# Kernel optimization log

Hardware: AMD Instinct MI355X
Metric: run time of the kernel (lower is better)

Reference implementation:

```python
import jax, jax.numpy as jnp
import numpy as np

B, Q, D, H, HD = 16, 300, 256, 8, 32
LV, P, NL, FF, NC = 3, 4, 6, 1024, 80
SPATIAL = ((80, 80), (40, 40), (20, 20))
LEN = sum(h * w for h, w in SPATIAL)  # 8400


def _layer_norm(x, g, b):
    m = jnp.mean(x, -1, keepdims=True)
    v = jnp.mean((x - m) ** 2, -1, keepdims=True)
    return (x - m) * jax.lax.rsqrt(v + 1e-5) * g + b


def _inverse_sigmoid(x, eps=1e-5):
    x = jnp.clip(x, eps, 1.0 - eps)
    return jnp.log(x / (1.0 - x))


def _bilinear(img, x, y, Hl, Wl):
    # img: (B*H, C, Hl*Wl); x, y: (B*H, N) pixel coords; matches
    # F.grid_sample(align_corners=False, padding_mode='zeros')
    x0 = jnp.floor(x)
    y0 = jnp.floor(y)
    wx1 = x - x0
    wy1 = y - y0

    def g(xi, yi, w):
        valid = (xi >= 0) & (xi <= Wl - 1) & (yi >= 0) & (yi <= Hl - 1)
        idx = jnp.clip(yi, 0, Hl - 1).astype(jnp.int32) * Wl + jnp.clip(xi, 0, Wl - 1).astype(jnp.int32)
        idxb = jnp.broadcast_to(idx[:, None, :], (img.shape[0], img.shape[1], idx.shape[-1]))
        v = jnp.take_along_axis(img, idxb, axis=2)
        return v * (w * valid)[:, None, :]

    return (g(x0, y0, (1 - wx1) * (1 - wy1)) + g(x0 + 1, y0, wx1 * (1 - wy1))
            + g(x0, y0 + 1, (1 - wx1) * wy1) + g(x0 + 1, y0 + 1, wx1 * wy1))


def _msda(query, ref, value, oW, ob, aW, ab, OW, Ob):
    # query: (B,Q,D); ref: (B,Q,4) in [0,1]; value: (B,LEN,H,HD)
    off = (query @ oW + ob).reshape(B, Q, H, LV, P, 2)
    aw = jax.nn.softmax((query @ aW + ab).reshape(B, Q, H, LV * P), -1).reshape(B, Q, H, LV, P)
    loc = ref[:, :, None, None, None, :2] + off / P * ref[:, :, None, None, None, 2:] * 0.5
    out = jnp.zeros((B, Q, H, HD), query.dtype)
    start = 0
    for l, (Hl, Wl) in enumerate(SPATIAL):
        img = value[:, start:start + Hl * Wl].transpose(0, 2, 3, 1).reshape(B * H, HD, Hl * Wl)
        start += Hl * Wl
        gl = loc[:, :, :, l].transpose(0, 2, 1, 3, 4).reshape(B * H, Q * P, 2)
        s = _bilinear(img, gl[..., 0] * Wl - 0.5, gl[..., 1] * Hl - 0.5, Hl, Wl).reshape(B, H, HD, Q, P)
        out = out + jnp.einsum('bhdqp,bqhp->bqhd', s, aw[:, :, :, l])
    return out.reshape(B, Q, D) @ OW + Ob


def _mha(qx, kx, vx, Wq, bq, Wk, bk, Wv, bv, Wo, bo):
    q = (qx @ Wq + bq).reshape(B, Q, H, HD)
    k = (kx @ Wk + bk).reshape(B, Q, H, HD)
    v = (vx @ Wv + bv).reshape(B, Q, H, HD)
    a = jax.nn.softmax(jnp.einsum('bqhd,bkhd->bhqk', q, k) * np.float32(1.0 / np.sqrt(HD)), -1)
    return jnp.einsum('bhqk,bkhd->bqhd', a, v).reshape(B, Q, D) @ Wo + bo


def _core(tgt, ref_points_unact, memory, self_Wq, self_bq, self_Wk, self_bk, self_Wv, self_bv, self_Wo, self_bo, ln1_g, ln1_b, ln2_g, ln2_b, ln3_g, ln3_b, off_W, off_b, aw_W, aw_b, val_W, val_b, out_W, out_b, ffn_W1, ffn_b1, ffn_W2, ffn_b2, qph_W1, qph_b1, qph_W2, qph_b2, bb_W1, bb_b1, bb_W2, bb_b2, bb_W3, bb_b3, sc_W, sc_b):
    out = tgt
    ref = jax.nn.sigmoid(ref_points_unact)
    for i in range(NL):
        qpe = jax.nn.relu(ref @ qph_W1 + qph_b1) @ qph_W2 + qph_b2
        q = out + qpe
        out = _layer_norm(out + _mha(q, q, out, self_Wq[i], self_bq[i], self_Wk[i], self_bk[i], self_Wv[i], self_bv[i], self_Wo[i], self_bo[i]), ln1_g[i], ln1_b[i])
        value = (memory @ val_W[i] + val_b[i]).reshape(B, LEN, H, HD)
        out = _layer_norm(out + _msda(out + qpe, ref, value, off_W[i], off_b[i], aw_W[i], aw_b[i], out_W[i], out_b[i]), ln2_g[i], ln2_b[i])
        ff = jax.nn.relu(out @ ffn_W1[i] + ffn_b1[i]) @ ffn_W2[i] + ffn_b2[i]
        out = _layer_norm(out + ff, ln3_g[i], ln3_b[i])
        bb = jax.nn.relu(out @ bb_W1[i] + bb_b1[i])
        bb = jax.nn.relu(bb @ bb_W2[i] + bb_b2[i])
        bb = bb @ bb_W3[i] + bb_b3[i]
        ref = jax.nn.sigmoid(bb + _inverse_sigmoid(ref))
    logits = out @ sc_W[NL - 1] + sc_b[NL - 1]
    return ref, logits


def setup_inputs():
    ks = iter(jax.random.split(jax.random.key(0), 48))

    def rn(shape, s=0.02):
        return jax.random.normal(next(ks), shape, jnp.float32) * s

    z = lambda shape: jnp.zeros(shape, jnp.float32)
    o = lambda shape: jnp.ones(shape, jnp.float32)
    L = NL
    return {
        'tgt': rn((B, Q, D), 1.0),
        'ref_points_unact': rn((B, Q, 4), 1.0),
        'memory': rn((B, LEN, D), 1.0),
        'memory_spatial_shapes': jnp.array(SPATIAL, jnp.int32),
        'self_Wq': rn((L, D, D)), 'self_bq': z((L, D)),
        'self_Wk': rn((L, D, D)), 'self_bk': z((L, D)),
        'self_Wv': rn((L, D, D)), 'self_bv': z((L, D)),
        'self_Wo': rn((L, D, D)), 'self_bo': z((L, D)),
        'ln1_g': o((L, D)), 'ln1_b': z((L, D)),
        'ln2_g': o((L, D)), 'ln2_b': z((L, D)),
        'ln3_g': o((L, D)), 'ln3_b': z((L, D)),
        'off_W': rn((L, D, H * LV * P * 2)), 'off_b': rn((L, H * LV * P * 2), 0.5),
        'aw_W': rn((L, D, H * LV * P)), 'aw_b': z((L, H * LV * P)),
        'val_W': rn((L, D, D)), 'val_b': z((L, D)),
        'out_W': rn((L, D, D)), 'out_b': z((L, D)),
        'ffn_W1': rn((L, D, FF)), 'ffn_b1': z((L, FF)),
        'ffn_W2': rn((L, FF, D)), 'ffn_b2': z((L, D)),
        'qph_W1': rn((4, 2 * D)), 'qph_b1': z((2 * D,)),
        'qph_W2': rn((2 * D, D)), 'qph_b2': z((D,)),
        'bb_W1': rn((L, D, D)), 'bb_b1': z((L, D)),
        'bb_W2': rn((L, D, D)), 'bb_b2': z((L, D)),
        'bb_W3': rn((L, D, 4)), 'bb_b3': z((L, 4)),
        'sc_W': rn((L, D, NC)), 'sc_b': z((L, NC)),
    }


def reference(tgt, ref_points_unact, memory, memory_spatial_shapes, self_Wq, self_bq, self_Wk, self_bk, self_Wv, self_bv, self_Wo, self_bo, ln1_g, ln1_b, ln2_g, ln2_b, ln3_g, ln3_b, off_W, off_b, aw_W, aw_b, val_W, val_b, out_W, out_b, ffn_W1, ffn_b1, ffn_W2, ffn_b2, qph_W1, qph_b1, qph_W2, qph_b2, bb_W1, bb_b1, bb_W2, bb_b2, bb_W3, bb_b3, sc_W, sc_b):
    # memory_spatial_shapes must equal SPATIAL (static constants under jit)
    ref, logits = _core(tgt, ref_points_unact, memory, self_Wq, self_bq, self_Wk, self_bk, self_Wv, self_bv, self_Wo, self_bo, ln1_g, ln1_b, ln2_g, ln2_b, ln3_g, ln3_b, off_W, off_b, aw_W, aw_b, val_W, val_b, out_W, out_b, ffn_W1, ffn_b1, ffn_W2, ffn_b2, qph_W1, qph_b1, qph_W2, qph_b2, bb_W1, bb_b1, bb_W2, bb_b2, bb_W3, bb_b3, sc_W, sc_b)
    # eval path: stacked outputs from the eval_idx (last) layer
    return (ref[None], logits[None])
```

## Files before the change

kernel.cpp:

```cpp
#include <hip/hip_runtime.h>

#define DI __device__ __forceinline__

typedef __attribute__((ext_vector_type(8))) short short8;
typedef __attribute__((ext_vector_type(4))) float f32x4;
typedef unsigned short u16;

DI u16 f2bf(float f) {
    union { float f; unsigned u; } v; v.f = f;
    unsigned u = v.u;
    return (u16)((u + 0x7fffu + ((u >> 16) & 1u)) >> 16);
}
DI float bf2f(u16 h) {
    union { unsigned u; float f; } v; v.u = ((unsigned)h) << 16;
    return v.f;
}
DI int lds_off(int row, int slot) {
    return row * 64 + (((slot ^ ((row >> 1) & 3)) << 4));
}

__global__ __launch_bounds__(256) void k_wt(const float* __restrict__ W, u16* __restrict__ Wt,
                                            int K, int N, int dstL)
{
    __shared__ u16 t[32][33];
    const int tid = threadIdx.x;
    const int kt = blockIdx.x * 32, nt = blockIdx.y * 32;
    const float* Wl = W + (size_t)blockIdx.z * K * N;
    u16* Wtl = Wt + (size_t)blockIdx.z * dstL;
#pragma unroll
    for (int i = 0; i < 4; i++) {
        int k = kt + (tid >> 5) + i * 8;
        int n = nt + (tid & 31);
        float v = (n < N) ? Wl[(size_t)k * N + n] : 0.f;
        t[tid & 31][(tid >> 5) + i * 8] = f2bf(v);
    }
    __syncthreads();
#pragma unroll
    for (int i = 0; i < 4; i++) {
        int n = nt + (tid >> 5) + i * 8;
        int k = kt + (tid & 31);
        if (n < N) Wtl[(size_t)n * K + k] = t[(tid >> 5) + i * 8][tid & 31];
    }
}

__global__ void k_packbias(const float* __restrict__ a, const float* __restrict__ b,
                           int na, int nb, float* __restrict__ dst)
{
    int i = blockIdx.x * 256 + threadIdx.x;
    int L = blockIdx.z;
    float* d = dst + (size_t)L * (na + nb);
    if (i < na) d[i] = a[(size_t)L * na + i];
    if (i < nb) d[na + i] = b[(size_t)L * nb + i];
}

template<int TM, int AMODE, int STORE, bool RELU, bool RESID>
__global__ __launch_bounds__(256) void k_gemm(
    const void* __restrict__ Ap, const float* __restrict__ A2,
    const u16* __restrict__ Bt, const float* __restrict__ bias,
    const float* __restrict__ resid, void* __restrict__ Cp,
    int M, int N, int K)
{
    constexpr int MI = TM / 32;
    __shared__ alignas(16) char Asm[TM * 64];
    __shared__ alignas(16) char Bsm[128 * 64];
    const int tid  = threadIdx.x;
    const int lane = tid & 63;
    const int wave = tid >> 6;
    const int wr = wave >> 1, wc = wave & 1;
    const int m0 = blockIdx.x * TM, n0 = blockIdx.y * 128;

    f32x4 acc[MI][4] = {};

    for (int kb = 0; kb < K; kb += 32) {
        if (AMODE == 2) {
            const u16* A = (const u16*)Ap;
            int r = tid >> 2, ko = (tid & 3) << 3;
            int grow = m0 + r; if (grow > M - 1) grow = M - 1;
            uint4 v = *(const uint4*)(A + (size_t)grow * K + kb + ko);
            *(uint4*)(Asm + lds_off(r, ko >> 3)) = v;
        } else {
            constexpr int AIT = (TM * 8) / 256;
#pragma unroll
            for (int j = 0; j < AIT; j++) {
                int flat = tid + j * 256;
                int r = flat >> 3, kq = flat & 7;
                int grow = m0 + r; if (grow > M - 1) grow = M - 1;
                const float* p = (const float*)Ap + (size_t)grow * K + kb + (kq << 2);
                float4 v = *(const float4*)p;
                if (AMODE == 1) {
                    float4 w = *(const float4*)(A2 + (size_t)grow * K + kb + (kq << 2));
                    v.x += w.x; v.y += w.y; v.z += w.z; v.w += w.w;
                }
                ushort4 h; h.x = f2bf(v.x); h.y = f2bf(v.y); h.z = f2bf(v.z); h.w = f2bf(v.w);
                *(ushort4*)(Asm + lds_off(r, kq >> 1) + ((kq & 1) << 3)) = h;
            }
        }
#pragma unroll
        for (int j = 0; j < 2; j++) {
            int item = tid + j * 256;
            int n = item >> 2, kq = item & 3;
            int gn = n0 + n; if (gn > N - 1) gn = N - 1;
            uint4 v = *(const uint4*)(Bt + (size_t)gn * K + kb + (kq << 3));
            *(uint4*)(Bsm + lds_off(n, kq)) = v;
        }
        __syncthreads();

        short8 af[MI], bfr[4];
#pragma unroll
        for (int mi = 0; mi < MI; mi++) {
            int r = wr * (TM / 2) + (mi << 4) + (lane & 15);
            af[mi] = *(const short8*)(Asm + lds_off(r, lane >> 4));
        }
#pragma unroll
        for (int ni = 0; ni < 4; ni++) {
            int c = (wc << 6) + (ni << 4) + (lane & 15);
            bfr[ni] = *(const short8*)(Bsm + lds_off(c, lane >> 4));
        }
#pragma unroll
        for (int mi = 0; mi < MI; mi++)
#pragma unroll
            for (int ni = 0; ni < 4; ni++)
                acc[mi][ni] = __builtin_amdgcn_mfma_f32_16x16x32_bf16(af[mi], bfr[ni], acc[mi][ni], 0, 0, 0);
        __syncthreads();
    }

    const int cl = lane & 15, rb = (lane >> 4) << 2;
#pragma unroll
    for (int mi = 0; mi < MI; mi++) {
#pragma unroll
        for (int ni = 0; ni < 4; ni++) {
            int col = n0 + (wc << 6) + (ni << 4) + cl;
            if (col >= N) continue;
            float bv = bias[col];
#pragma unroll
            for (int e = 0; e < 4; e++) {
                int row = m0 + wr * (TM / 2) + (mi << 4) + rb + e;
                if (row >= M) continue;
                float v = acc[mi][ni][e] + bv;
                if (RESID) v += resid[(size_t)row * N + col];
                if (RELU)  v = fmaxf(v, 0.f);
                if (STORE == 0) {
                    ((float*)Cp)[(size_t)row * N + col] = v;
                } else {
                    int b = row / 8400, pix = row - b * 8400;
                    int h = col >> 5, hd = col & 31;
                    ((u16*)Cp)[(((size_t)(b * 8 + h)) * 8400 + pix) * 32 + hd] = f2bf(v);
                }
            }
        }
    }
}

__global__ __launch_bounds__(256) void k_mha3(const float* __restrict__ qk, const float* __restrict__ Vp,
                                              float* __restrict__ outp)
{
    __shared__ alignas(16) char lds[62976];
    u16* Ksh = (u16*)lds;
    u16* Psh = (u16*)lds;
    u16* Vt  = (u16*)(lds + 41984);

    const int q0 = blockIdx.x * 64;
    const int bh = blockIdx.y;
    const int h = bh & 7, b = bh >> 3;
    const int tid = threadIdx.x;
    const int wv = tid >> 6, l = tid & 63;
    const int c15 = l & 15, slot = l >> 4;
    const float scale = 0.17677669529663687f;

    for (int item = tid; item < 304 * 8; item += 256) {
        int kk = item >> 3, dq = (item & 7) << 2;
        ushort4 hv = {0, 0, 0, 0};
        if (kk < 300) {
            float4 v = *(const float4*)(qk + (size_t)(b * 300 + kk) * 512 + 256 + h * 32 + dq);
            hv.x = f2bf(v.x); hv.y = f2bf(v.y); hv.z = f2bf(v.z); hv.w = f2bf(v.w);
        }
        *(ushort4*)(Ksh + kk * 40 + dq) = hv;
    }
    for (int item = tid; item < 320 * 8; item += 256) {
        int kk = item >> 3, dq = (item & 7) << 2;
        float4 v = {0, 0, 0, 0};
        if (kk < 300)
            v = *(const float4*)(Vp + (size_t)(b * 300 + kk) * 256 + h * 32 + dq);
        Vt[(dq + 0) * 328 + kk] = f2bf(v.x);
        Vt[(dq + 1) * 328 + kk] = f2bf(v.y);
        Vt[(dq + 2) * 328 + kk] = f2bf(v.z);
        Vt[(dq + 3) * 328 + kk] = f2bf(v.w);
    }
    short8 qf;
    {
        int qrow = q0 + 16 * wv + c15; if (qrow > 299) qrow = 299;
        const float* qs = qk + (size_t)(b * 300 + qrow) * 512 + h * 32 + (slot << 3);
        float4 a0 = *(const float4*)qs, a1 = *(const float4*)(qs + 4);
        qf[0] = (short)f2bf(a0.x * scale); qf[1] = (short)f2bf(a0.y * scale);
        qf[2] = (short)f2bf(a0.z * scale); qf[3] = (short)f2bf(a0.w * scale);
        qf[4] = (short)f2bf(a1.x * scale); qf[5] = (short)f2bf(a1.y * scale);
        qf[6] = (short)f2bf(a1.z * scale); qf[7] = (short)f2bf(a1.w * scale);
    }
    __syncthreads();

    f32x4 sc[19];
    const f32x4 zero4 = {0.f, 0.f, 0.f, 0.f};
#pragma unroll
    for (int t = 0; t < 19; t++) {
        short8 kf = *(const short8*)(Ksh + (16 * t + c15) * 40 + (slot << 3));
        sc[t] = __builtin_amdgcn_mfma_f32_16x16x32_bf16(qf, kf, zero4, 0, 0, 0);
    }
    __syncthreads();

    float linv[4];
    const int prow0 = 16 * wv + (slot << 2);
#pragma unroll
    for (int e = 0; e < 4; e++) {
        float mm = -1e30f;
#pragma unroll
        for (int t = 0; t < 18; t++) mm = fmaxf(mm, sc[t][e]);
        if (c15 < 12) mm = fmaxf(mm, sc[18][e]);
        mm = fmaxf(mm, __shfl_xor(mm, 1));
        mm = fmaxf(mm, __shfl_xor(mm, 2));
        mm = fmaxf(mm, __shfl_xor(mm, 4));
        mm = fmaxf(mm, __shfl_xor(mm, 8));
        float ls = 0.f;
#pragma unroll
        for (int t = 0; t < 19; t++) {
            float p = __expf(sc[t][e] - mm);
            if (t == 18 && c15 >= 12) p = 0.f;
            ls += p;
            Psh[(prow0 + e) * 328 + 16 * t + c15] = f2bf(p);
        }
        ls += __shfl_xor(ls, 1);
        ls += __shfl_xor(ls, 2);
        ls += __shfl_xor(ls, 4);
        ls += __shfl_xor(ls, 8);
        linv[e] = 1.f / ls;
    }
    {
        int r = 16 * wv + (l >> 2);
        int c = 304 + ((l & 3) << 2);
        Psh[r * 328 + c + 0] = 0; Psh[r * 328 + c + 1] = 0;
        Psh[r * 328 + c + 2] = 0; Psh[r * 328 + c + 3] = 0;
    }

#pragma unroll
    for (int df = 0; df < 2; df++) {
        f32x4 o = zero4;
#pragma unroll
        for (int t = 0; t < 10; t++) {
            short8 pf = *(const short8*)(Psh + (16 * wv + c15) * 328 + 32 * t + (slot << 3));
            short8 vf = *(const short8*)(Vt + (16 * df + c15) * 328 + 32 * t + (slot << 3));
            o = __builtin_amdgcn_mfma_f32_16x16x32_bf16(pf, vf, o, 0, 0, 0);
        }
#pragma unroll
        for (int e = 0; e < 4; e++) {
            int qrow = q0 + prow0 + e;
            if (qrow < 300)
                outp[(size_t)(b * 300 + qrow) * 256 + h * 32 + 16 * df + c15] = o[e] * linv[e];
        }
    }
}

__global__ __launch_bounds__(256) void k_ln(const float* __restrict__ x, const float* __restrict__ g,
                                            const float* __restrict__ bb, float* __restrict__ out, int M)
{
    int row = blockIdx.x * 4 + (threadIdx.x >> 6);
    int lane = threadIdx.x & 63;
    if (row >= M) return;
    const float* xr = x + (size_t)row * 256;
    float4 v = *(const float4*)(xr + lane * 4);
    float s  = v.x + v.y + v.z + v.w;
    float s2 = v.x*v.x + v.y*v.y + v.z*v.z + v.w*v.w;
#pragma unroll
    for (int off = 32; off >= 1; off >>= 1) {
        s  += __shfl_xor(s, off);
        s2 += __shfl_xor(s2, off);
    }
    float m   = s * 0.00390625f;
    float var = s2 * 0.00390625f - m * m;
    float r   = rsqrtf(var + 1e-5f);
    float4 gv = *(const float4*)(g + lane * 4);
    float4 bv = *(const float4*)(bb + lane * 4);
    float4 o;
    o.x = (v.x - m) * r * gv.x + bv.x;
    o.y = (v.y - m) * r * gv.y + bv.y;
    o.z = (v.z - m) * r * gv.z + bv.z;
    o.w = (v.w - m) * r * gv.w + bv.w;
    *(float4*)(out + (size_t)row * 256 + lane * 4) = o;
}

__global__ void k_awsm(float* __restrict__ offaw, int n)
{
    int g = blockIdx.x * 256 + threadIdx.x;
    if (g >= n) return;
    int row = g >> 3, h = g & 7;
    float* p = offaw + (size_t)row * 288 + 192 + h * 12;
    float m = p[0];
#pragma unroll
    for (int i = 1; i < 12; i++) m = fmaxf(m, p[i]);
    float e[12]; float s = 0.f;
#pragma unroll
    for (int i = 0; i < 12; i++) { e[i] = __expf(p[i] - m); s += e[i]; }
    float inv = 1.f / s;
#pragma unroll
    for (int i = 0; i < 12; i++) p[i] = e[i] * inv;
}

__global__ __launch_bounds__(256) void k_msda(const u16* __restrict__ value, const float* __restrict__ offaw,
                                              const float* __restrict__ ref, float* __restrict__ samp)
{
    int it = blockIdx.x * 8 + (threadIdx.x >> 5);
    int d  = threadIdx.x & 31;
    int h = it & 7, row = it >> 3;
    int b = row / 300;
    const float* rf = ref + (size_t)row * 4;
    float rx = rf[0], ry = rf[1];
    float rw = rf[2] * 0.125f, rh = rf[3] * 0.125f;
    const float* offp = offaw + (size_t)row * 288 + h * 24;
    const float* awp  = offaw + (size_t)row * 288 + 192 + h * 12;
    const u16* vb = value + ((size_t)(b * 8 + h)) * 8400 * 32 + d;
    const int HW[3] = {80, 40, 20};
    const int st[3] = {0, 6400, 8000};
    float acc = 0.f;
#pragma unroll
    for (int lv = 0; lv < 3; lv++) {
        int Wl = HW[lv], Hl = HW[lv];
        float Wf = (float)Wl, Hf = (float)Hl;
#pragma unroll
        for (int p = 0; p < 4; p++) {
            float a = awp[lv * 4 + p];
            float x = (rx + offp[lv*8 + p*2]     * rw) * Wf - 0.5f;
            float y = (ry + offp[lv*8 + p*2 + 1] * rh) * Hf - 0.5f;
            float xf = floorf(x), yf = floorf(y);
            float wx = x - xf, wy = y - yf;
            int x0 = (int)xf, y0 = (int)yf;
#pragma unroll
            for (int t = 0; t < 4; t++) {
                int xx = x0 + (t & 1), yy = y0 + (t >> 1);
                if (xx >= 0 && xx < Wl && yy >= 0 && yy < Hl) {
                    float w = ((t & 1) ? wx : 1.f - wx) * ((t >> 1) ? wy : 1.f - wy);
                    acc += a * w * bf2f(vb[(size_t)(st[lv] + yy * Wl + xx) * 32]);
                }
            }
        }
    }
    samp[(size_t)row * 256 + h * 32 + d] = acc;
}

__global__ void k_qpe_hidden(const float* __restrict__ ref, const float* __restrict__ W1,
                             const float* __restrict__ b1, float* __restrict__ hid)
{
    int idx = blockIdx.x * 256 + threadIdx.x;
    if (idx >= 4800 * 512) return;
    int row = idx >> 9, col = idx & 511;
    const float* r = ref + (size_t)row * 4;
    float v = b1[col] + r[0]*W1[col] + r[1]*W1[512+col] + r[2]*W1[1024+col] + r[3]*W1[1536+col];
    hid[idx] = fmaxf(v, 0.f);
}

__global__ __launch_bounds__(64) void k_bb3(const float* __restrict__ bb2, const float* __restrict__ W3,
                                            const float* __restrict__ b3, float* __restrict__ ref)
{
    int row = blockIdx.x;
    int lane = threadIdx.x;
    const float* xr = bb2 + (size_t)row * 256;
    float s0 = 0, s1 = 0, s2 = 0, s3 = 0;
#pragma unroll
    for (int k = lane; k < 256; k += 64) {
        float xv = xr[k];
        float4 w = *(const float4*)(W3 + k * 4);
        s0 += xv * w.x; s1 += xv * w.y; s2 += xv * w.z; s3 += xv * w.w;
    }
#pragma unroll
    for (int off = 32; off >= 1; off >>= 1) {
        s0 += __shfl_xor(s0, off); s1 += __shfl_xor(s1, off);
        s2 += __shfl_xor(s2, off); s3 += __shfl_xor(s3, off);
    }
    if (lane == 0) {
        float sv[4] = {s0, s1, s2, s3};
        float* rr = ref + (size_t)row * 4;
#pragma unroll
        for (int j = 0; j < 4; j++) {
            float v = sv[j] + b3[j];
            float o = rr[j];
            o = fminf(fmaxf(o, 1e-5f), 1.f - 1e-5f);
            float inv = logf(o / (1.f - o));
            rr[j] = 1.f / (1.f + expf(-(v + inv)));
        }
    }
}

__global__ void k_cvt_bf16(const float* __restrict__ in, u16* __restrict__ out, int n4)
{
    int i = blockIdx.x * 256 + threadIdx.x;
    if (i >= n4) return;
    float4 v = ((const float4*)in)[i];
    ushort4 h; h.x = f2bf(v.x); h.y = f2bf(v.y); h.z = f2bf(v.z); h.w = f2bf(v.w);
    ((ushort4*)out)[i] = h;
}
__global__ void k_copy4(const float* __restrict__ in, float* __restrict__ out, int n4)
{
    int i = blockIdx.x * 256 + threadIdx.x;
    if (i >= n4) return;
    ((float4*)out)[i] = ((const float4*)in)[i];
}
__global__ void k_sigmoid(const float* __restrict__ in, float* __restrict__ out, int n)
{
    int i = blockIdx.x * 256 + threadIdx.x;
    if (i >= n) return;
    out[i] = 1.f / (1.f + __expf(-in[i]));
}

static inline dim3 g32(int M, int N) { return dim3((M + 31) / 32, (N + 127) / 128); }

static void gemm_plain(const float* A, const u16* Bt, const float* bias, float* C,
                       int M, int N, int K, hipStream_t s) {
    k_gemm<32, 0, 0, false, false><<<g32(M, N), 256, 0, s>>>((const void*)A, nullptr, Bt, bias, nullptr, (void*)C, M, N, K);
}
static void gemm_add(const float* A, const float* A2, const u16* Bt, const float* bias, float* C,
                     int M, int N, int K, hipStream_t s) {
    k_gemm<32, 1, 0, false, false><<<g32(M, N), 256, 0, s>>>((const void*)A, A2, Bt, bias, nullptr, (void*)C, M, N, K);
}
static void gemm_resid(const float* A, const u16* Bt, const float* bias, const float* resid, float* C,
                       int M, int N, int K, hipStream_t s) {
    k_gemm<32, 0, 0, false, true><<<g32(M, N), 256, 0, s>>>((const void*)A, nullptr, Bt, bias, resid, (void*)C, M, N, K);
}
static void gemm_relu(const float* A, const u16* Bt, const float* bias, float* C,
                      int M, int N, int K, hipStream_t s) {
    k_gemm<32, 0, 0, true, false><<<g32(M, N), 256, 0, s>>>((const void*)A, nullptr, Bt, bias, nullptr, (void*)C, M, N, K);
}
static void gemm_value(const u16* A, const u16* Bt, const float* bias, u16* C, hipStream_t s) {
    k_gemm<64, 2, 1, false, false><<<dim3(2100, 2), 256, 0, s>>>((const void*)A, nullptr, Bt, bias, nullptr, (void*)C, 134400, 256, 256);
}

extern "C" void kernel_launch(void* const* d_in, const int* in_sizes, int n_in,
                              void* d_out, int out_size, void* d_ws, size_t ws_size,
                              hipStream_t stream)
{
    const float* tgt       = (const float*)d_in[0];
    const float* ref_unact = (const float*)d_in[1];
    const float* memory    = (const float*)d_in[2];
    const float* self_Wq = (const float*)d_in[4];
    const float* self_bq = (const float*)d_in[5];
    const float* self_Wk = (const float*)d_in[6];
    const float* self_bk = (const float*)d_in[7];
    const float* self_Wv = (const float*)d_in[8];
    const float* self_bv = (const float*)d_in[9];
    const float* self_Wo = (const float*)d_in[10];
    const float* self_bo = (const float*)d_in[11];
    const float* ln1_g = (const float*)d_in[12];
    const float* ln1_b = (const float*)d_in[13];
    const float* ln2_g = (const float*)d_in[14];
    const float* ln2_b = (const float*)d_in[15];
    const float* ln3_g = (const float*)d_in[16];
    const float* ln3_b = (const float*)d_in[17];
    const float* off_W = (const float*)d_in[18];
    const float* off_b = (const float*)d_in[19];
    const float* aw_W  = (const float*)d_in[20];
    const float* aw_b  = (const float*)d_in[21];
    const float* val_W = (const float*)d_in[22];
    const float* val_b = (const float*)d_in[23];
    const float* out_W = (const float*)d_in[24];
    const float* out_b = (const float*)d_in[25];
    const float* ffn_W1 = (const float*)d_in[26];
    const float* ffn_b1 = (const float*)d_in[27];
    const float* ffn_W2 = (const float*)d_in[28];
    const float* ffn_b2 = (const float*)d_in[29];
    const float* qph_W1 = (const float*)d_in[30];
    const float* qph_b1 = (const float*)d_in[31];
    const float* qph_W2 = (const float*)d_in[32];
    const float* qph_b2 = (const float*)d_in[33];
    const float* bb_W1 = (const float*)d_in[34];
    const float* bb_b1 = (const float*)d_in[35];
    const float* bb_W2 = (const float*)d_in[36];
    const float* bb_b2 = (const float*)d_in[37];
    const float* bb_W3 = (const float*)d_in[38];
    const float* bb_b3 = (const float*)d_in[39];
    const float* sc_W  = (const float*)d_in[40];
    const float* sc_b  = (const float*)d_in[41];
    float* out_f = (float*)d_out;

    char* w = (char*)d_ws;
    u16* mem_bf = (u16*)(w + 0);
    u16* value  = (u16*)(w + 68812800);
    const size_t F0 = 137625600;
    float* ws_out   = (float*)(w + F0);
    float* ws_tmp   = (float*)(w + F0 +  4915200);
    float* ws_qpe   = (float*)(w + F0 +  9830400);
    float* ws_hid   = (float*)(w + F0 + 14745600);
    float* ws_qk    = (float*)(w + F0 + 24576000);
    float* ws_v     = (float*)(w + F0 + 34406400);
    float* ws_attn  = (float*)(w + F0 + 39321600);
    float* ws_offaw = (float*)(w + F0 + 44236800);
    float* ws_samp  = (float*)(w + F0 + 49766400);
    float* ws_ffn   = (float*)(w + F0 + 54681600);
    float* ws_bb1   = (float*)(w + F0 + 74342400);
    float* ws_bb2   = (float*)(w + F0 + 79257600);
    float* ws_ref   = (float*)(w + F0 + 84172800);
    float* bias_qk  = (float*)(w + F0 + 84256800);
    float* bias_oa  = (float*)(w + F0 + 84269088);
    u16* wt = (u16*)(w + F0 + 84276000);
    u16* wt_qk    = wt;
    u16* wt_v     = wt_qk    + 786432;
    u16* wt_o     = wt_v     + 393216;
    u16* wt_offaw = wt_o     + 393216;
    u16* wt_val   = wt_offaw + 442368;
    u16* wt_out   = wt_val   + 393216;
    u16* wt_f1    = wt_out   + 393216;
    u16* wt_f2    = wt_f1    + 1572864;
    u16* wt_b1    = wt_f2    + 1572864;
    u16* wt_b2    = wt_b1    + 393216;
    u16* wt_qp2   = wt_b2    + 393216;
    u16* wt_sc    = wt_qp2   + 131072;

    k_wt<<<dim3(8, 8, 6),  256, 0, stream>>>(self_Wq, wt_qk,            256, 256, 131072);
    k_wt<<<dim3(8, 8, 6),  256, 0, stream>>>(self_Wk, wt_qk + 65536,    256, 256, 131072);
    k_wt<<<dim3(8, 8, 6),  256, 0, stream>>>(self_Wv, wt_v,             256, 256, 65536);
    k_wt<<<dim3(8, 8, 6),  256, 0, stream>>>(self_Wo, wt_o,             256, 256, 65536);
    k_wt<<<dim3(8, 6, 6),  256, 0, stream>>>(off_W,   wt_offaw,         256, 192, 73728);
    k_wt<<<dim3(8, 3, 6),  256, 0, stream>>>(aw_W,    wt_offaw + 49152, 256, 96,  73728);
    k_wt<<<dim3(8, 8, 6),  256, 0, stream>>>(val_W,   wt_val,           256, 256, 65536);
    k_wt<<<dim3(8, 8, 6),  256, 0, stream>>>(out_W,   wt_out,           256, 256, 65536);
    k_wt<<<dim3(8, 32, 6), 256, 0, stream>>>(ffn_W1,  wt_f1,            256, 1024, 262144);
    k_wt<<<dim3(32, 8, 6), 256, 0, stream>>>(ffn_W2,  wt_f2,            1024, 256, 262144);
    k_wt<<<dim3(8, 8, 6),  256, 0, stream>>>(bb_W1,   wt_b1,            256, 256, 65536);
    k_wt<<<dim3(8, 8, 6),  256, 0, stream>>>(bb_W2,   wt_b2,            256, 256, 65536);
    k_wt<<<dim3(16, 8, 1), 256, 0, stream>>>(qph_W2,  wt_qp2,           512, 256, 131072);
    k_wt<<<dim3(8, 3, 1),  256, 0, stream>>>(sc_W + (size_t)5 * 20480, wt_sc, 256, 80, 20480);
    k_packbias<<<dim3(1, 1, 6), 256, 0, stream>>>(self_bq, self_bk, 256, 256, bias_qk);
    k_packbias<<<dim3(1, 1, 6), 256, 0, stream>>>(off_b, aw_b, 192, 96, bias_oa);

    k_cvt_bf16<<<33600, 256, 0, stream>>>(memory, mem_bf, 8601600);
    k_copy4   <<<1200,  256, 0, stream>>>(tgt, ws_out, 307200);
    k_sigmoid <<<75,    256, 0, stream>>>(ref_unact, ws_ref, 19200);

    for (int l = 0; l < 6; l++) {
        k_qpe_hidden<<<9600, 256, 0, stream>>>(ws_ref, qph_W1, qph_b1, ws_hid);
        gemm_plain(ws_hid, wt_qp2, qph_b2, ws_qpe, 4800, 256, 512, stream);

        gemm_add(ws_out, ws_qpe, wt_qk + (size_t)l * 131072, bias_qk + l * 512, ws_qk, 4800, 512, 256, stream);
        gemm_plain(ws_out, wt_v + (size_t)l * 65536, self_bv + l * 256, ws_v, 4800, 256, 256, stream);
        k_mha3<<<dim3(5, 128), 256, 0, stream>>>(ws_qk, ws_v, ws_attn);
        gemm_resid(ws_attn, wt_o + (size_t)l * 65536, self_bo + l * 256, ws_out, ws_tmp, 4800, 256, 256, stream);
        k_ln<<<1200, 256, 0, stream>>>(ws_tmp, ln1_g + l * 256, ln1_b + l * 256, ws_out, 4800);

        gemm_value(mem_bf, wt_val + (size_t)l * 65536, val_b + l * 256, value, stream);

        gemm_add(ws_out, ws_qpe, wt_offaw + (size_t)l * 73728, bias_oa + l * 288, ws_offaw, 4800, 288, 256, stream);
        k_awsm<<<150, 256, 0, stream>>>(ws_offaw, 38400);
        k_msda<<<4800, 256, 0, stream>>>(value, ws_offaw, ws_ref, ws_samp);
        gemm_resid(ws_samp, wt_out + (size_t)l * 65536, out_b + l * 256, ws_out, ws_tmp, 4800, 256, 256, stream);
        k_ln<<<1200, 256, 0, stream>>>(ws_tmp, ln2_g + l * 256, ln2_b + l * 256, ws_out, 4800);

        gemm_relu(ws_out, wt_f1 + (size_t)l * 262144, ffn_b1 + l * 1024, ws_ffn, 4800, 1024, 256, stream);
        gemm_resid(ws_ffn, wt_f2 + (size_t)l * 262144, ffn_b2 + l * 256, ws_out, ws_tmp, 4800, 256, 1024, stream);
        k_ln<<<1200, 256, 0, stream>>>(ws_tmp, ln3_g + l * 256, ln3_b + l * 256, ws_out, 4800);

        gemm_relu(ws_out, wt_b1 + (size_t)l * 65536, bb_b1 + l * 256, ws_bb1, 4800, 256, 256, stream);
        gemm_relu(ws_bb1, wt_b2 + (size_t)l * 65536, bb_b2 + l * 256, ws_bb2, 4800, 256, 256, stream);
        k_bb3<<<4800, 64, 0, stream>>>(ws_bb2, bb_W3 + (size_t)l * 1024, bb_b3 + l * 4, ws_ref);
    }

    k_copy4<<<19, 256, 0, stream>>>(ws_ref, out_f, 4800);
    gemm_plain(ws_out, wt_sc, sc_b + 5 * 80, out_f + 19200, 4800, 80, 256, stream);
}
```

Baseline: 2.208 ms.

## Fuse QKV projection, GEMM+residual+LayerNorm, softmax into MSDA; enlarge value-GEMM tile

Measured after the change: 2.333 ms. 5.7% more time.

```diff
diff --git a/kernel.cpp b/kernel.cpp
--- a/kernel.cpp
+++ b/kernel.cpp
@@ -43,14 +43,12 @@
     }
 }
 
-__global__ void k_packbias(const float* __restrict__ a, const float* __restrict__ b,
-                           int na, int nb, float* __restrict__ dst)
+__global__ void k_packb(const float* __restrict__ src, int n, float* __restrict__ dst,
+                        int off, int dstL)
 {
     int i = blockIdx.x * 256 + threadIdx.x;
     int L = blockIdx.z;
-    float* d = dst + (size_t)L * (na + nb);
-    if (i < na) d[i] = a[(size_t)L * na + i];
-    if (i < nb) d[na + i] = b[(size_t)L * nb + i];
+    if (i < n) dst[(size_t)L * dstL + off + i] = src[(size_t)L * n + i];
 }
 
 template<int TM, int AMODE, int STORE, bool RELU, bool RESID>
@@ -68,16 +66,21 @@
     const int wave = tid >> 6;
     const int wr = wave >> 1, wc = wave & 1;
     const int m0 = blockIdx.x * TM, n0 = blockIdx.y * 128;
+    const bool addA2 = (AMODE == 1) || (AMODE == 3 && n0 < 512);
 
     f32x4 acc[MI][4] = {};
 
     for (int kb = 0; kb < K; kb += 32) {
         if (AMODE == 2) {
             const u16* A = (const u16*)Ap;
-            int r = tid >> 2, ko = (tid & 3) << 3;
-            int grow = m0 + r; if (grow > M - 1) grow = M - 1;
-            uint4 v = *(const uint4*)(A + (size_t)grow * K + kb + ko);
-            *(uint4*)(Asm + lds_off(r, ko >> 3)) = v;
+#pragma unroll
+            for (int j = 0; j < (TM * 4) / 256; j++) {
+                int item = tid + j * 256;
+                int r = item >> 2, ko = (item & 3) << 3;
+                int grow = m0 + r; if (grow > M - 1) grow = M - 1;
+                uint4 v = *(const uint4*)(A + (size_t)grow * K + kb + ko);
+                *(uint4*)(Asm + lds_off(r, ko >> 3)) = v;
+            }
         } else {
             constexpr int AIT = (TM * 8) / 256;
 #pragma unroll
@@ -87,7 +90,7 @@
                 int grow = m0 + r; if (grow > M - 1) grow = M - 1;
                 const float* p = (const float*)Ap + (size_t)grow * K + kb + (kq << 2);
                 float4 v = *(const float4*)p;
-                if (AMODE == 1) {
+                if (addA2) {
                     float4 w = *(const float4*)(A2 + (size_t)grow * K + kb + (kq << 2));
                     v.x += w.x; v.y += w.y; v.z += w.z; v.w += w.w;
                 }
@@ -151,8 +154,94 @@
     }
 }
 
-__global__ __launch_bounds__(256) void k_mha3(const float* __restrict__ qk, const float* __restrict__ Vp,
-                                              float* __restrict__ outp)
+__global__ __launch_bounds__(256) void k_gemm_ln(
+    const float* __restrict__ Ap, const u16* __restrict__ Bt, const float* __restrict__ bias,
+    const float* __restrict__ resid, const float* __restrict__ g, const float* __restrict__ bb,
+    float* __restrict__ outp, int M, int K)
+{
+    __shared__ alignas(16) char lds[17408];
+    char* Asm = lds;
+    char* Bsm = lds + 1024;
+    float* Cf = (float*)lds;
+    const int tid = threadIdx.x;
+    const int lane = tid & 63;
+    const int wc = tid >> 6;
+    const int c15 = lane & 15, slot = lane >> 4;
+    const int m0 = blockIdx.x * 16;
+
+    f32x4 acc[4] = {};
+
+    for (int kb = 0; kb < K; kb += 32) {
+        if (tid < 128) {
+            int r = tid >> 3, kq = tid & 7;
+            const float* p = Ap + (size_t)(m0 + r) * K + kb + (kq << 2);
+            float4 v = *(const float4*)p;
+            ushort4 h; h.x = f2bf(v.x); h.y = f2bf(v.y); h.z = f2bf(v.z); h.w = f2bf(v.w);
+            *(ushort4*)(Asm + lds_off(r, kq >> 1) + ((kq & 1) << 3)) = h;
+        }
+#pragma unroll
+        for (int j = 0; j < 4; j++) {
+            int item = tid + j * 256;
+            int n = item >> 2, kq = item & 3;
+            uint4 v = *(const uint4*)(Bt + (size_t)n * K + kb + (kq << 3));
+            *(uint4*)(Bsm + lds_off(n, kq)) = v;
+        }
+        __syncthreads();
+
+        short8 af = *(const short8*)(Asm + lds_off(c15, slot));
+#pragma unroll
+        for (int ni = 0; ni < 4; ni++) {
+            int c = (wc << 6) + (ni << 4) + c15;
+            short8 bfr = *(const short8*)(Bsm + lds_off(c, slot));
+            acc[ni] = __builtin_amdgcn_mfma_f32_16x16x32_bf16(af, bfr, acc[ni], 0, 0, 0);
+        }
+        __syncthreads();
+    }
+
+#pragma unroll
+    for (int ni = 0; ni < 4; ni++) {
+        int col = (wc << 6) + (ni << 4) + c15;
+        float bv = bias[col];
+#pragma unroll
+        for (int e = 0; e < 4; e++) {
+            int rowl = (slot << 2) + e;
+            float v = acc[ni][e] + bv + resid[(size_t)(m0 + rowl) * 256 + col];
+            Cf[rowl * 264 + col] = v;
+        }
+    }
+    __syncthreads();
+
+    const int row = tid >> 4, l16 = tid & 15;
+    float s = 0.f, s2 = 0.f;
+#pragma unroll
+    for (int j = 0; j < 16; j++) {
+        float x = Cf[row * 264 + l16 + j * 16];
+        s += x; s2 += x * x;
+    }
+    s  += __shfl_xor(s, 1);  s2 += __shfl_xor(s2, 1);
+    s  += __shfl_xor(s, 2);  s2 += __shfl_xor(s2, 2);
+    s  += __shfl_xor(s, 4);  s2 += __shfl_xor(s2, 4);
+    s  += __shfl_xor(s, 8);  s2 += __shfl_xor(s2, 8);
+    float m   = s * 0.00390625f;
+    float var = s2 * 0.00390625f - m * m;
+    float r   = rsqrtf(var + 1e-5f);
+    float* orow = outp + (size_t)(m0 + row) * 256;
+#pragma unroll
+    for (int j = 0; j < 4; j++) {
+        int c = j * 64 + l16 * 4;
+        float4 x = *(const float4*)(Cf + row * 264 + c);
+        float4 gv = *(const float4*)(g + c);
+        float4 bv = *(const float4*)(bb + c);
+        float4 o;
+        o.x = (x.x - m) * r * gv.x + bv.x;
+        o.y = (x.y - m) * r * gv.y + bv.y;
+        o.z = (x.z - m) * r * gv.z + bv.z;
+        o.w = (x.w - m) * r * gv.w + bv.w;
+        *(float4*)(orow + c) = o;
+    }
+}
+
+__global__ __launch_bounds__(256) void k_mha3(const float* __restrict__ qkv, float* __restrict__ outp)
 {
     __shared__ alignas(16) char lds[62976];
     u16* Ksh = (u16*)lds;
@@ -171,7 +260,7 @@
         int kk = item >> 3, dq = (item & 7) << 2;
         ushort4 hv = {0, 0, 0, 0};
         if (kk < 300) {
-            float4 v = *(const float4*)(qk + (size_t)(b * 300 + kk) * 512 + 256 + h * 32 + dq);
+            float4 v = *(const float4*)(qkv + (size_t)(b * 300 + kk) * 768 + 256 + h * 32 + dq);
             hv.x = f2bf(v.x); hv.y = f2bf(v.y); hv.z = f2bf(v.z); hv.w = f2bf(v.w);
         }
         *(ushort4*)(Ksh + kk * 40 + dq) = hv;
@@ -180,7 +269,7 @@
         int kk = item >> 3, dq = (item & 7) << 2;
         float4 v = {0, 0, 0, 0};
         if (kk < 300)
-            v = *(const float4*)(Vp + (size_t)(b * 300 + kk) * 256 + h * 32 + dq);
+            v = *(const float4*)(qkv + (size_t)(b * 300 + kk) * 768 + 512 + h * 32 + dq);
         Vt[(dq + 0) * 328 + kk] = f2bf(v.x);
         Vt[(dq + 1) * 328 + kk] = f2bf(v.y);
         Vt[(dq + 2) * 328 + kk] = f2bf(v.z);
@@ -189,7 +278,7 @@
     short8 qf;
     {
         int qrow = q0 + 16 * wv + c15; if (qrow > 299) qrow = 299;
-        const float* qs = qk + (size_t)(b * 300 + qrow) * 512 + h * 32 + (slot << 3);
+        const float* qs = qkv + (size_t)(b * 300 + qrow) * 768 + h * 32 + (slot << 3);
         float4 a0 = *(const float4*)qs, a1 = *(const float4*)(qs + 4);
         qf[0] = (short)f2bf(a0.x * scale); qf[1] = (short)f2bf(a0.y * scale);
         qf[2] = (short)f2bf(a0.z * scale); qf[3] = (short)f2bf(a0.w * scale);
@@ -256,51 +345,6 @@
                 outp[(size_t)(b * 300 + qrow) * 256 + h * 32 + 16 * df + c15] = o[e] * linv[e];
         }
     }
-}
-
-__global__ __launch_bounds__(256) void k_ln(const float* __restrict__ x, const float* __restrict__ g,
-                                            const float* __restrict__ bb, float* __restrict__ out, int M)
-{
-    int row = blockIdx.x * 4 + (threadIdx.x >> 6);
-    int lane = threadIdx.x & 63;
-    if (row >= M) return;
-    const float* xr = x + (size_t)row * 256;
-    float4 v = *(const float4*)(xr + lane * 4);
-    float s  = v.x + v.y + v.z + v.w;
-    float s2 = v.x*v.x + v.y*v.y + v.z*v.z + v.w*v.w;
-#pragma unroll
-    for (int off = 32; off >= 1; off >>= 1) {
-        s  += __shfl_xor(s, off);
-        s2 += __shfl_xor(s2, off);
-    }
-    float m   = s * 0.00390625f;
-    float var = s2 * 0.00390625f - m * m;
-    float r   = rsqrtf(var + 1e-5f);
-    float4 gv = *(const float4*)(g + lane * 4);
-    float4 bv = *(const float4*)(bb + lane * 4);
-    float4 o;
-    o.x = (v.x - m) * r * gv.x + bv.x;
-    o.y = (v.y - m) * r * gv.y + bv.y;
-    o.z = (v.z - m) * r * gv.z + bv.z;
-    o.w = (v.w - m) * r * gv.w + bv.w;
-    *(float4*)(out + (size_t)row * 256 + lane * 4) = o;
-}
-
-__global__ void k_awsm(float* __restrict__ offaw, int n)
-{
-    int g = blockIdx.x * 256 + threadIdx.x;
-    if (g >= n) return;
-    int row = g >> 3, h = g & 7;
-    float* p = offaw + (size_t)row * 288 + 192 + h * 12;
-    float m = p[0];
-#pragma unroll
-    for (int i = 1; i < 12; i++) m = fmaxf(m, p[i]);
-    float e[12]; float s = 0.f;
-#pragma unroll
-    for (int i = 0; i < 12; i++) { e[i] = __expf(p[i] - m); s += e[i]; }
-    float inv = 1.f / s;
-#pragma unroll
-    for (int i = 0; i < 12; i++) p[i] = e[i] * inv;
 }
 
 __global__ __launch_bounds__(256) void k_msda(const u16* __restrict__ value, const float* __restrict__ offaw,
@@ -315,6 +359,18 @@
     float rw = rf[2] * 0.125f, rh = rf[3] * 0.125f;
     const float* offp = offaw + (size_t)row * 288 + h * 24;
     const float* awp  = offaw + (size_t)row * 288 + 192 + h * 12;
+    float aw[12];
+    {
+        float mm = awp[0];
+#pragma unroll
+        for (int i = 1; i < 12; i++) mm = fmaxf(mm, awp[i]);
+        float ssum = 0.f;
+#pragma unroll
+        for (int i = 0; i < 12; i++) { aw[i] = __expf(awp[i] - mm); ssum += aw[i]; }
+        float inv = 1.f / ssum;
+#pragma unroll
+        for (int i = 0; i < 12; i++) aw[i] *= inv;
+    }
     const u16* vb = value + ((size_t)(b * 8 + h)) * 8400 * 32 + d;
     const int HW[3] = {80, 40, 20};
     const int st[3] = {0, 6400, 8000};
@@ -325,7 +381,7 @@
         float Wf = (float)Wl, Hf = (float)Hl;
 #pragma unroll
         for (int p = 0; p < 4; p++) {
-            float a = awp[lv * 4 + p];
+            float a = aw[lv * 4 + p];
             float x = (rx + offp[lv*8 + p*2]     * rw) * Wf - 0.5f;
             float y = (ry + offp[lv*8 + p*2 + 1] * rh) * Hf - 0.5f;
             float xf = floorf(x), yf = floorf(y);
@@ -418,16 +474,20 @@
                      int M, int N, int K, hipStream_t s) {
     k_gemm<32, 1, 0, false, false><<<g32(M, N), 256, 0, s>>>((const void*)A, A2, Bt, bias, nullptr, (void*)C, M, N, K);
 }
-static void gemm_resid(const float* A, const u16* Bt, const float* bias, const float* resid, float* C,
-                       int M, int N, int K, hipStream_t s) {
-    k_gemm<32, 0, 0, false, true><<<g32(M, N), 256, 0, s>>>((const void*)A, nullptr, Bt, bias, resid, (void*)C, M, N, K);
+static void gemm_qkv(const float* A, const float* A2, const u16* Bt, const float* bias, float* C,
+                     hipStream_t s) {
+    k_gemm<32, 3, 0, false, false><<<g32(4800, 768), 256, 0, s>>>((const void*)A, A2, Bt, bias, nullptr, (void*)C, 4800, 768, 256);
 }
 static void gemm_relu(const float* A, const u16* Bt, const float* bias, float* C,
                       int M, int N, int K, hipStream_t s) {
     k_gemm<32, 0, 0, true, false><<<g32(M, N), 256, 0, s>>>((const void*)A, nullptr, Bt, bias, nullptr, (void*)C, M, N, K);
 }
 static void gemm_value(const u16* A, const u16* Bt, const float* bias, u16* C, hipStream_t s) {
-    k_gemm<64, 2, 1, false, false><<<dim3(2100, 2), 256, 0, s>>>((const void*)A, nullptr, Bt, bias, nullptr, (void*)C, 134400, 256, 256);
+    k_gemm<128, 2, 1, false, false><<<dim3(1050, 2), 256, 0, s>>>((const void*)A, nullptr, Bt, bias, nullptr, (void*)C, 134400, 256, 256);
+}
+static void gemm_ln(const float* A, const u16* Bt, const float* bias, const float* resid,
+                    const float* g, const float* bb, float* out, int K, hipStream_t s) {
+    k_gemm_ln<<<300, 256, 0, s>>>(A, Bt, bias, resid, g, bb, out, 4800, K);
 }
 
 extern "C" void kernel_launch(void* const* d_in, const int* in_sizes, int n_in,
@@ -482,24 +542,21 @@
     u16* value  = (u16*)(w + 68812800);
     const size_t F0 = 137625600;
     float* ws_out   = (float*)(w + F0);
-    float* ws_tmp   = (float*)(w + F0 +  4915200);
-    float* ws_qpe   = (float*)(w + F0 +  9830400);
-    float* ws_hid   = (float*)(w + F0 + 14745600);
-    float* ws_qk    = (float*)(w + F0 + 24576000);
-    float* ws_v     = (float*)(w + F0 + 34406400);
-    float* ws_attn  = (float*)(w + F0 + 39321600);
-    float* ws_offaw = (float*)(w + F0 + 44236800);
-    float* ws_samp  = (float*)(w + F0 + 49766400);
-    float* ws_ffn   = (float*)(w + F0 + 54681600);
-    float* ws_bb1   = (float*)(w + F0 + 74342400);
-    float* ws_bb2   = (float*)(w + F0 + 79257600);
-    float* ws_ref   = (float*)(w + F0 + 84172800);
-    float* bias_qk  = (float*)(w + F0 + 84256800);
-    float* bias_oa  = (float*)(w + F0 + 84269088);
-    u16* wt = (u16*)(w + F0 + 84276000);
-    u16* wt_qk    = wt;
-    u16* wt_v     = wt_qk    + 786432;
-    u16* wt_o     = wt_v     + 393216;
+    float* ws_qpe   = (float*)(w + F0 +  4915200);
+    float* ws_hid   = (float*)(w + F0 +  9830400);
+    float* ws_qkv   = (float*)(w + F0 + 19660800);
+    float* ws_attn  = (float*)(w + F0 + 34406400);
+    float* ws_offaw = (float*)(w + F0 + 39321600);
+    float* ws_samp  = (float*)(w + F0 + 44851200);
+    float* ws_ffn   = (float*)(w + F0 + 49766400);
+    float* ws_bb1   = (float*)(w + F0 + 69427200);
+    float* ws_bb2   = (float*)(w + F0 + 74342400);
+    float* ws_ref   = (float*)(w + F0 + 79257600);
+    float* bias_qkv = (float*)(w + F0 + 79334400);
+    float* bias_oa  = (float*)(w + F0 + 79352832);
+    u16* wt = (u16*)(w + F0 + 79360000);
+    u16* wt_qkv   = wt;
+    u16* wt_o     = wt_qkv   + 1179648;
     u16* wt_offaw = wt_o     + 393216;
     u16* wt_val   = wt_offaw + 442368;
     u16* wt_out   = wt_val   + 393216;
@@ -510,9 +567,9 @@
     u16* wt_qp2   = wt_b2    + 393216;
     u16* wt_sc    = wt_qp2   + 131072;
 
-    k_wt<<<dim3(8, 8, 6),  256, 0, stream>>>(self_Wq, wt_qk,            256, 256, 131072);
-    k_wt<<<dim3(8, 8, 6),  256, 0, stream>>>(self_Wk, wt_qk + 65536,    256, 256, 131072);
-    k_wt<<<dim3(8, 8, 6),  256, 0, stream>>>(self_Wv, wt_v,             256, 256, 65536);
+    k_wt<<<dim3(8, 8, 6),  256, 0, stream>>>(self_Wq, wt_qkv,           256, 256, 196608);
+    k_wt<<<dim3(8, 8, 6),  256, 0, stream>>>(self_Wk, wt_qkv + 65536,   256, 256, 196608);
+    k_wt<<<dim3(8, 8, 6),  256, 0, stream>>>(self_Wv, wt_qkv + 131072,  256, 256, 196608);
     k_wt<<<dim3(8, 8, 6),  256, 0, stream>>>(self_Wo, wt_o,             256, 256, 65536);
     k_wt<<<dim3(8, 6, 6),  256, 0, stream>>>(off_W,   wt_offaw,         256, 192, 73728);
     k_wt<<<dim3(8, 3, 6),  256, 0, stream>>>(aw_W,    wt_offaw + 49152, 256, 96,  73728);
@@ -524,8 +581,11 @@
     k_wt<<<dim3(8, 8, 6),  256, 0, stream>>>(bb_W2,   wt_b2,            256, 256, 65536);
     k_wt<<<dim3(16, 8, 1), 256, 0, stream>>>(qph_W2,  wt_qp2,           512, 256, 131072);
     k_wt<<<dim3(8, 3, 1),  256, 0, stream>>>(sc_W + (size_t)5 * 20480, wt_sc, 256, 80, 20480);
-    k_packbias<<<dim3(1, 1, 6), 256, 0, stream>>>(self_bq, self_bk, 256, 256, bias_qk);
-    k_packbias<<<dim3(1, 1, 6), 256, 0, stream>>>(off_b, aw_b, 192, 96, bias_oa);
+    k_packb<<<dim3(1, 1, 6), 256, 0, stream>>>(self_bq, 256, bias_qkv, 0,   768);
+    k_packb<<<dim3(1, 1, 6), 256, 0, stream>>>(self_bk, 256, bias_qkv, 256, 768);
+    k_packb<<<dim3(1, 1, 6), 256, 0, stream>>>(self_bv, 256, bias_qkv, 512, 768);
+    k_packb<<<dim3(1, 1, 6), 256, 0, stream>>>(off_b,   192, bias_oa,  0,   288);
+    k_packb<<<dim3(1, 1, 6), 256, 0, stream>>>(aw_b,     96, bias_oa,  192, 288);
 
     k_cvt_bf16<<<33600, 256, 0, stream>>>(memory, mem_bf, 8601600);
     k_copy4   <<<1200,  256, 0, stream>>>(tgt, ws_out, 307200);
@@ -535,23 +595,21 @@
         k_qpe_hidden<<<9600, 256, 0, stream>>>(ws_ref, qph_W1, qph_b1, ws_hid);
         gemm_plain(ws_hid, wt_qp2, qph_b2, ws_qpe, 4800, 256, 512, stream);
 
-        gemm_add(ws_out, ws_qpe, wt_qk + (size_t)l * 131072, bias_qk + l * 512, ws_qk, 4800, 512, 256, stream);
-        gemm_plain(ws_out, wt_v + (size_t)l * 65536, self_bv + l * 256, ws_v, 4800, 256, 256, stream);
-        k_mha3<<<dim3(5, 128), 256, 0, stream>>>(ws_qk, ws_v, ws_attn);
-        gemm_resid(ws_attn, wt_o + (size_t)l * 65536, self_bo + l * 256, ws_out, ws_tmp, 4800, 256, 256, stream);
-        k_ln<<<1200, 256, 0, stream>>>(ws_tmp, ln1_g + l * 256, ln1_b + l * 256, ws_out, 4800);
+        gemm_qkv(ws_out, ws_qpe, wt_qkv + (size_t)l * 196608, bias_qkv + l * 768, ws_qkv, stream);
+        k_mha3<<<dim3(5, 128), 256, 0, stream>>>(ws_qkv, ws_attn);
+        gemm_ln(ws_attn, wt_o + (size_t)l * 65536, self_bo + l * 256, ws_out,
+                ln1_g + l * 256, ln1_b + l * 256, ws_out, 256, stream);
 
         gemm_value(mem_bf, wt_val + (size_t)l * 65536, val_b + l * 256, value, stream);
 
         gemm_add(ws_out, ws_qpe, wt_offaw + (size_t)l * 73728, bias_oa + l * 288, ws_offaw, 4800, 288, 256, stream);
-        k_awsm<<<150, 256, 0, stream>>>(ws_offaw, 38400);
         k_msda<<<4800, 256, 0, stream>>>(value, ws_offaw, ws_ref, ws_samp);
-        gemm_resid(ws_samp, wt_out + (size_t)l * 65536, out_b + l * 256, ws_out, ws_tmp, 4800, 256, 256, stream);
-        k_ln<<<1200, 256, 0, stream>>>(ws_tmp, ln2_g + l * 256, ln2_b + l * 256, ws_out, 4800);
+        gemm_ln(ws_samp, wt_out + (size_t)l * 65536, out_b + l * 256, ws_out,
+                ln2_g + l * 256, ln2_b + l * 256, ws_out, 256, stream);
 
         gemm_relu(ws_out, wt_f1 + (size_t)l * 262144, ffn_b1 + l * 1024, ws_ffn, 4800, 1024, 256, stream);
-        gemm_resid(ws_ffn, wt_f2 + (size_t)l * 262144, ffn_b2 + l * 256, ws_out, ws_tmp, 4800, 256, 1024, stream);
-        k_ln<<<1200, 256, 0, stream>>>(ws_tmp, ln3_g + l * 256, ln3_b + l * 256, ws_out, 4800);
+        gemm_ln(ws_ffn, wt_f2 + (size_t)l * 262144, ffn_b2 + l * 256, ws_out,
+                ln3_g + l * 256, ln3_b + l * 256, ws_out, 1024, stream);
 
         gemm_relu(ws_out, wt_b1 + (size_t)l * 65536, bb_b1 + l * 256, ws_bb1, 4800, 256, 256, stream);
         gemm_relu(ws_bb1, wt_b2 + (size_t)l * 65536, bb_b2 + l * 256, ws_bb2, 4800, 256, 256, stream);
```
